# Kernel tuning notes

Measured on AMD Instinct MI355X. Metric: run time of the kernel, lower is better.

Reference implementation:

```python
import jax, jax.numpy as jnp
import numpy as np

D_MODEL = 1024
N_HEADS = 16
N_KV_HEADS = 4
D_K = D_MODEL // N_HEADS
Q_SIZE = D_MODEL
KV_SIZE = N_KV_HEADS * D_K
QKV_SIZE = Q_SIZE + 2 * KV_SIZE
EPS = 1.1920929e-07  # torch.nn.RMSNorm default eps (fp32 machine eps)
ROPE_BASE = 10000.0


def rms_norm(x, w):
    # normalize over last dim, learned scale (torch nn.RMSNorm)
    return x * jax.lax.rsqrt(jnp.mean(x * x, axis=-1, keepdims=True) + EPS) * w


def rope(x):
    # torchtune RotaryPositionalEmbeddings: interleaved pairs, x is [B,T,H,D]
    T, d = x.shape[1], x.shape[-1]
    inv_freq = 1.0 / (ROPE_BASE ** (jnp.arange(0, d, 2, dtype=jnp.float32) / d))
    ang = jnp.arange(T, dtype=jnp.float32)[:, None] * inv_freq[None, :]  # [T, d/2]
    cos = jnp.cos(ang)[None, :, None, :]
    sin = jnp.sin(ang)[None, :, None, :]
    xr = x.reshape(x.shape[:-1] + (d // 2, 2))
    x1, x2 = xr[..., 0], xr[..., 1]
    out = jnp.stack([x1 * cos - x2 * sin, x1 * sin + x2 * cos], axis=-1)
    return out.reshape(x.shape)


def setup_inputs() -> dict:
    key = jax.random.key(0)
    k1, k2 = jax.random.split(key)
    x = jax.random.normal(k1, (2, 2048, D_MODEL), dtype=jnp.float32)
    qkvo = jax.random.normal(k2, (QKV_SIZE + D_MODEL, D_MODEL), dtype=jnp.float32) * 0.02
    q_norm_w = jnp.ones((D_K,), dtype=jnp.float32)
    k_norm_w = jnp.ones((D_K,), dtype=jnp.float32)
    return {"x": x, "qkvo": qkvo, "q_norm_w": q_norm_w, "k_norm_w": k_norm_w}


def reference(x, qkvo, q_norm_w, k_norm_w):
    B, T, _ = x.shape
    groups = N_HEADS // N_KV_HEADS
    qkv = x @ qkvo[:QKV_SIZE].T  # [B,T,qkv_size]
    Q = qkv[..., :Q_SIZE].reshape(B, T, N_HEADS, D_K)
    K = qkv[..., Q_SIZE:Q_SIZE + KV_SIZE].reshape(B, T, N_KV_HEADS, D_K)
    V = qkv[..., Q_SIZE + KV_SIZE:].reshape(B, T, N_KV_HEADS, D_K)
    Q = rope(rms_norm(Q, q_norm_w))
    K = rope(rms_norm(K, k_norm_w))
    K = jnp.repeat(K, groups, axis=2)  # GQA expand to [B,T,H,D]
    V = jnp.repeat(V, groups, axis=2)
    scale = 1.0 / np.sqrt(D_K).astype(np.float32)
    scores = jnp.einsum('bqhd,bkhd->bhqk', Q, K) * scale
    causal = jnp.tril(jnp.ones((T, T), dtype=bool))
    scores = jnp.where(causal[None, None], scores, jnp.float32(-jnp.inf))
    attn = jax.nn.softmax(scores, axis=-1)
    out = jnp.einsum('bhqk,bkhd->bqhd', attn, V).reshape(B, T, D_MODEL)
    return out @ qkvo[QKV_SIZE:].T
```

## Files before the change

### kernel.cpp

```cpp
#include <hip/hip_runtime.h>
#include <hip/hip_bf16.h>
#include <cstdint>
#include <cstddef>

typedef __bf16 bf16x8 __attribute__((ext_vector_type(8)));
typedef float f32x4 __attribute__((ext_vector_type(4)));

__device__ __forceinline__ unsigned short f2bf(float f) {
    unsigned u = __builtin_bit_cast(unsigned, f);
    u += 0x7FFFu + ((u >> 16) & 1u);
    return (unsigned short)(u >> 16);
}
__device__ __forceinline__ unsigned pk2(float a, float b) {
    typedef __bf16 bf16x2 __attribute__((ext_vector_type(2)));
    bf16x2 h;
    h[0] = (__bf16)a;
    h[1] = (__bf16)b;
    unsigned r;
    __builtin_memcpy(&r, &h, 4);
    return r;
}
__device__ __forceinline__ float fexp2(float x) {
#if __has_builtin(__builtin_amdgcn_exp2f)
    return __builtin_amdgcn_exp2f(x);
#else
    return __expf(x * 0.6931471805599453f);
#endif
}
__device__ __forceinline__ void gld16(const void* g, void* l) {
    __builtin_amdgcn_global_load_lds((const __attribute__((address_space(1))) void*)g,
                                     (__attribute__((address_space(3))) void*)l, 16, 0, 0);
}

__global__ __launch_bounds__(256) void cast_kernel(const float4* __restrict__ x,
                                                   const float4* __restrict__ w,
                                                   ushort4* __restrict__ xbf,
                                                   ushort4* __restrict__ wbf) {
    int i = blockIdx.x * 256 + threadIdx.x;
    const int NX4 = 4096 * 1024 / 4;
    const int NW4 = 2560 * 1024 / 4;
    float4 v;
    ushort4* o;
    if (i < NX4) { v = x[i]; o = xbf + i; }
    else {
        int j = i - NX4;
        if (j >= NW4) return;
        v = w[j]; o = wbf + j;
    }
    ushort4 r;
    r.x = f2bf(v.x); r.y = f2bf(v.y); r.z = f2bf(v.z); r.w = f2bf(v.w);
    *o = r;
}

__global__ __launch_bounds__(256) void gemm_bf16(const ushort* __restrict__ A,
                                                 const ushort* __restrict__ B,
                                                 float* __restrict__ C,
                                                 int M, int N, int K) {
    __shared__ __align__(16) ushort LA[2][8192];
    __shared__ __align__(16) ushort LB[2][8192];
    int tid = threadIdx.x;
    int w = tid >> 6, lane = tid & 63;
    int qm = lane & 15, quad = lane >> 4;
    int m0 = blockIdx.x * 128, n0 = blockIdx.y * 128;
    int mw = (w & 1) * 64, nw = (w >> 1) * 64;
    int sw = qm & 7;

    f32x4 acc[4][4];
#pragma unroll
    for (int i = 0; i < 4; i++)
#pragma unroll
        for (int j = 0; j < 4; j++) acc[i][j] = (f32x4){0.f, 0.f, 0.f, 0.f};

    int s[4], rr[4], gg[4];
#pragma unroll
    for (int u = 0; u < 4; u++) {
        s[u] = tid + u * 256;
        rr[u] = s[u] >> 3;
        gg[u] = (s[u] & 7) ^ (rr[u] & 7);
    }

    auto do_stage = [&](int k0, int buf) {
#pragma unroll
        for (int u = 0; u < 4; u++)
            gld16(A + (size_t)(m0 + rr[u]) * K + k0 + gg[u] * 8, &LA[buf][s[u] * 8]);
#pragma unroll
        for (int u = 0; u < 4; u++)
            gld16(B + (size_t)(n0 + rr[u]) * K + k0 + gg[u] * 8, &LB[buf][s[u] * 8]);
    };

    do_stage(0, 0);
    int buf = 0;
    for (int k0 = 0; k0 < K; k0 += 64, buf ^= 1) {
        __syncthreads();
        if (k0 + 64 < K) do_stage(k0 + 64, buf ^ 1);
        bf16x8 a[4][2], bb[4][2];
#pragma unroll
        for (int mi = 0; mi < 4; mi++)
#pragma unroll
            for (int h = 0; h < 2; h++)
                a[mi][h] = *(const bf16x8*)&LA[buf][((mw + mi * 16 + qm) * 8 + ((h * 4 + quad) ^ sw)) * 8];
#pragma unroll
        for (int ni = 0; ni < 4; ni++)
#pragma unroll
            for (int h = 0; h < 2; h++)
                bb[ni][h] = *(const bf16x8*)&LB[buf][((nw + ni * 16 + qm) * 8 + ((h * 4 + quad) ^ sw)) * 8];
#pragma unroll
        for (int h = 0; h < 2; h++)
#pragma unroll
            for (int mi = 0; mi < 4; mi++)
#pragma unroll
                for (int ni = 0; ni < 4; ni++)
                    acc[mi][ni] = __builtin_amdgcn_mfma_f32_16x16x32_bf16(a[mi][h], bb[ni][h], acc[mi][ni], 0, 0, 0);
    }
#pragma unroll
    for (int mi = 0; mi < 4; mi++)
#pragma unroll
        for (int ni = 0; ni < 4; ni++) {
            int row = m0 + mw + mi * 16 + quad * 4;
            int col = n0 + nw + ni * 16 + qm;
            float* cp = C + (size_t)row * N + col;
#pragma unroll
            for (int r = 0; r < 4; r++) cp[(size_t)r * N] = acc[mi][ni][r];
        }
}

__global__ __launch_bounds__(256) void normrope_kernel(const float* __restrict__ qkv,
                                                       const float* __restrict__ qw,
                                                       const float* __restrict__ kw,
                                                       ushort* __restrict__ Q,
                                                       ushort* __restrict__ Kb) {
    int r = blockIdx.x;
    int b = r >> 11;
    int t = r & 2047;
    int tid = threadIdx.x;
    int w = tid >> 6;
    int lane = tid & 63;

    float inv_freq = __expf(-((float)(lane & 62) * (1.0f / 64.0f)) * 9.210340371976184f);
    float sn, cs;
    sincosf((float)t * inv_freq, &sn, &cs);

#pragma unroll
    for (int hg = 0; hg < 5; hg++) {
        int col = hg * 256 + w * 64 + lane;
        float v = qkv[(size_t)r * 1536 + col];
        float ss = v * v;
#pragma unroll
        for (int m = 1; m < 64; m <<= 1) ss += __shfl_xor(ss, m);
        float rinv = rsqrtf(ss * (1.0f / 64.0f) + 1.1920929e-7f);
        float wt = (hg < 4) ? qw[lane] : kw[lane];
        float vn = v * rinv * wt;
        float pr = __shfl_xor(vn, 1);
        float out = (lane & 1) ? fmaf(pr, sn, vn * cs) : fmaf(vn, cs, -pr * sn);
        if (hg < 4) {
            int h = hg * 4 + w;
            Q[((size_t)(b * 16 + h) * 2048 + t) * 64 + lane] = f2bf(out * 0.125f);
        } else {
            Kb[((size_t)(b * 4 + w) * 2048 + t) * 64 + lane] = f2bf(out);
        }
    }
}

__global__ __launch_bounds__(256) void vtrans_kernel(const float* __restrict__ qkv,
                                                     ushort* __restrict__ VT) {
    __shared__ float tile[64][65];
    int bkv = blockIdx.x;
    int t0 = blockIdx.y * 64;
    int b = bkv >> 2;
    int kvh = bkv & 3;
    int tid = threadIdx.x;
    int c = tid & 63;
    int rr = tid >> 6;
#pragma unroll
    for (int p = 0; p < 16; p++) {
        int tl = p * 4 + rr;
        tile[tl][c] = qkv[((size_t)(b * 2048) + t0 + tl) * 1536 + 1280 + kvh * 64 + c];
    }
    __syncthreads();
#pragma unroll
    for (int p = 0; p < 16; p++) {
        int dd = p * 4 + rr;
        VT[((size_t)bkv * 64 + dd) * 2048 + t0 + c] = f2bf(tile[c][dd]);
    }
}

__global__ __launch_bounds__(256) void attn5_kernel(const ushort* __restrict__ Q,
                                                    const ushort* __restrict__ K,
                                                    const ushort* __restrict__ VT,
                                                    ushort* __restrict__ O) {
    __shared__ __align__(16) ushort KT[2][4096];
    __shared__ __align__(16) ushort VL[2][4096];
    __shared__ __align__(16) ushort PBuf[4][1024];

    const float LOG2E = 1.4426950408889634f;
    const float C8 = 11.541560327111707f;

    int blk = blockIdx.x;
    int bh = blk >> 4;
    int p  = blk & 15;
    int tid = threadIdx.x;
    int w = tid >> 6, lane = tid & 63;
    int qm = lane & 15, quad = lane >> 4;
    int b = bh >> 4, h = bh & 15;
    int bkv = b * 4 + (h >> 2);

    const ushort* Qbh = Q + (size_t)bh * 2048 * 64;
    const ushort* Kbh = K + (size_t)bkv * 2048 * 64;
    const ushort* Vbh = VT + (size_t)bkv * 64 * 2048;
    ushort* pb = PBuf[w];
    int sw = qm & 7;

    int s0 = tid, s1 = tid + 256;
    int r0 = s0 >> 3, g0 = (s0 & 7) ^ (r0 & 7);
    int r1 = s1 >> 3, g1 = (s1 & 7) ^ (r1 & 7);

    auto do_stage = [&](int j0, int buf) {
        gld16(Kbh + (size_t)(j0 + r0) * 64 + g0 * 8, &KT[buf][s0 * 8]);
        gld16(Kbh + (size_t)(j0 + r1) * 64 + g1 * 8, &KT[buf][s1 * 8]);
        gld16(Vbh + (size_t)r0 * 2048 + j0 + g0 * 8, &VL[buf][s0 * 8]);
        gld16(Vbh + (size_t)r1 * 2048 + j0 + g1 * 8, &VL[buf][s1 * 8]);
    };

    int qblkA = p, qblkB = 31 - p;
    int nchA = qblkA + 1;
    const int total = 33;

    int q0 = qblkA * 64 + w * 16;
    const ushort* qptr = Qbh + (size_t)(q0 + qm) * 64 + quad * 8;
    bf16x8 qb0 = *(const bf16x8*)qptr;
    bf16x8 qb1 = *(const bf16x8*)(qptr + 32);
    f32x4 oacc[4];
    float lacc = 0.f;
#pragma unroll
    for (int i = 0; i < 4; i++) oacc[i] = (f32x4){0.f, 0.f, 0.f, 0.f};

    auto writeO = [&]() {
        float l = lacc;
        l += __shfl_xor(l, 16);
        l += __shfl_xor(l, 32);
        float rinv = 1.0f / l;
        uint2 val;
#pragma unroll
        for (int dt = 0; dt < 4; dt++) {
            val.x = pk2(oacc[dt][0] * rinv, oacc[dt][1] * rinv);
            val.y = pk2(oacc[dt][2] * rinv, oacc[dt][3] * rinv);
            *(uint2*)&O[((size_t)(b * 2048) + q0 + qm) * 1024 + h * 64 + dt * 16 + quad * 4] = val;
        }
    };

    do_stage(0, 0);
    int buf = 0;
#pragma unroll 1
    for (int i = 0; i < total; i++, buf ^= 1) {
        bool inB = (i >= nchA);
        int c = inB ? i - nchA : i;
        int j0 = c * 64;
        int nch = inB ? (qblkB + 1) : nchA;

        if (i == nchA) {
            writeO();
            q0 = qblkB * 64 + w * 16;
            const ushort* qp2 = Qbh + (size_t)(q0 + qm) * 64 + quad * 8;
            qb0 = *(const bf16x8*)qp2;
            qb1 = *(const bf16x8*)(qp2 + 32);
            lacc = 0.f;
#pragma unroll
            for (int ii = 0; ii < 4; ii++) oacc[ii] = (f32x4){0.f, 0.f, 0.f, 0.f};
        }

        __syncthreads();
        int ni = i + 1;
        if (ni < total) do_stage(ni < nchA ? 64 * ni : 64 * (ni - nchA), buf ^ 1);

        f32x4 st[4];
#pragma unroll
        for (int tj = 0; tj < 4; tj++) st[tj] = (f32x4){0.f, 0.f, 0.f, 0.f};
#pragma unroll
        for (int tj = 0; tj < 4; tj++) {
            bf16x8 kf0 = *(const bf16x8*)&KT[buf][((16 * tj + qm) * 8 + (quad ^ sw)) * 8];
            bf16x8 kf1 = *(const bf16x8*)&KT[buf][((16 * tj + qm) * 8 + ((4 + quad) ^ sw)) * 8];
            st[tj] = __builtin_amdgcn_mfma_f32_16x16x32_bf16(kf0, qb0, st[tj], 0, 0, 0);
            st[tj] = __builtin_amdgcn_mfma_f32_16x16x32_bf16(kf1, qb1, st[tj], 0, 0, 0);
        }
        if (c == nch - 1) {
#pragma unroll
            for (int tj = 0; tj < 4; tj++)
#pragma unroll
                for (int r = 0; r < 4; r++) {
                    int key = j0 + tj * 16 + quad * 4 + r;
                    if (key > q0 + qm) st[tj][r] = -1e30f;
                }
        }
        float rs = 0.f;
#pragma unroll
        for (int tj = 0; tj < 4; tj++)
#pragma unroll
            for (int r = 0; r < 4; r++) {
                float pv = fexp2(fmaf(st[tj][r], LOG2E, -C8));
                st[tj][r] = pv;
                rs += pv;
            }
        lacc += rs;

#pragma unroll
        for (int tj = 0; tj < 4; tj++) {
            int g = 2 * tj + (quad >> 1);
            uint2 val;
            val.x = pk2(st[tj][0], st[tj][1]);
            val.y = pk2(st[tj][2], st[tj][3]);
            *(uint2*)&pb[(qm * 8 + (g ^ sw)) * 8 + (quad & 1) * 4] = val;
        }
        asm volatile("s_waitcnt lgkmcnt(0)" ::: "memory");

#pragma unroll
        for (int half = 0; half < 2; half++) {
            int gg = 4 * half + quad;
            bf16x8 pfrag = *(const bf16x8*)&pb[(qm * 8 + (gg ^ sw)) * 8];
#pragma unroll
            for (int dt = 0; dt < 4; dt++) {
                bf16x8 vf = *(const bf16x8*)&VL[buf][((16 * dt + qm) * 8 + (gg ^ sw)) * 8];
                oacc[dt] = __builtin_amdgcn_mfma_f32_16x16x32_bf16(vf, pfrag, oacc[dt], 0, 0, 0);
            }
        }
    }
    writeO();
}

extern "C" void kernel_launch(void* const* d_in, const int* in_sizes, int n_in,
                              void* d_out, int out_size, void* d_ws, size_t ws_size,
                              hipStream_t stream) {
    (void)in_sizes; (void)n_in; (void)out_size; (void)ws_size;
    const float* x    = (const float*)d_in[0];
    const float* qkvo = (const float*)d_in[1];
    const float* qw   = (const float*)d_in[2];
    const float* kw   = (const float*)d_in[3];
    float* out = (float*)d_out;

    char* ws = (char*)d_ws;
    ushort* xbf = (ushort*)(ws + 0);
    ushort* wbf = (ushort*)(ws + 8388608);
    float*  qkv = (float*)(ws + 13631488);
    ushort* Qb  = (ushort*)(ws + 38797312);
    ushort* Kb  = (ushort*)(ws + 47185920);
    ushort* VT  = (ushort*)(ws + 49283072);
    ushort* Ob  = (ushort*)(ws + 51380224);

    cast_kernel<<<6656, 256, 0, stream>>>((const float4*)x, (const float4*)qkvo,
                                          (ushort4*)xbf, (ushort4*)wbf);
    gemm_bf16<<<dim3(32, 12), 256, 0, stream>>>(xbf, wbf, qkv, 4096, 1536, 1024);
    normrope_kernel<<<4096, 256, 0, stream>>>(qkv, qw, kw, Qb, Kb);
    vtrans_kernel<<<dim3(8, 32), 256, 0, stream>>>(qkv, VT);
    attn5_kernel<<<512, 256, 0, stream>>>(Qb, Kb, VT, Ob);
    gemm_bf16<<<dim3(32, 8), 256, 0, stream>>>(Ob, wbf + (size_t)1536 * 1024, out, 4096, 1024, 1024);
}
```

Before: 171.8 us.

## Shrink GEMM M-tile to 64 and split attention into per-query-block workgroups

```diff
diff --git a/kernel.cpp b/kernel.cpp
--- a/kernel.cpp
+++ b/kernel.cpp
@@ -56,36 +56,43 @@
                                                  const ushort* __restrict__ B,
                                                  float* __restrict__ C,
                                                  int M, int N, int K) {
-    __shared__ __align__(16) ushort LA[2][8192];
+    __shared__ __align__(16) ushort LA[2][4096];
     __shared__ __align__(16) ushort LB[2][8192];
     int tid = threadIdx.x;
     int w = tid >> 6, lane = tid & 63;
     int qm = lane & 15, quad = lane >> 4;
-    int m0 = blockIdx.x * 128, n0 = blockIdx.y * 128;
-    int mw = (w & 1) * 64, nw = (w >> 1) * 64;
+    int m0 = blockIdx.x * 64, n0 = blockIdx.y * 128;
+    int mw = (w & 1) * 32, nw = (w >> 1) * 64;
     int sw = qm & 7;
 
-    f32x4 acc[4][4];
-#pragma unroll
-    for (int i = 0; i < 4; i++)
+    f32x4 acc[2][4];
+#pragma unroll
+    for (int i = 0; i < 2; i++)
 #pragma unroll
         for (int j = 0; j < 4; j++) acc[i][j] = (f32x4){0.f, 0.f, 0.f, 0.f};
 
-    int s[4], rr[4], gg[4];
+    int sa[2], ra[2], ga[2];
+#pragma unroll
+    for (int u = 0; u < 2; u++) {
+        sa[u] = tid + u * 256;
+        ra[u] = sa[u] >> 3;
+        ga[u] = (sa[u] & 7) ^ (ra[u] & 7);
+    }
+    int sb[4], rb[4], gb[4];
 #pragma unroll
     for (int u = 0; u < 4; u++) {
-        s[u] = tid + u * 256;
-        rr[u] = s[u] >> 3;
-        gg[u] = (s[u] & 7) ^ (rr[u] & 7);
+        sb[u] = tid + u * 256;
+        rb[u] = sb[u] >> 3;
+        gb[u] = (sb[u] & 7) ^ (rb[u] & 7);
     }
 
     auto do_stage = [&](int k0, int buf) {
 #pragma unroll
+        for (int u = 0; u < 2; u++)
+            gld16(A + (size_t)(m0 + ra[u]) * K + k0 + ga[u] * 8, &LA[buf][sa[u] * 8]);
+#pragma unroll
         for (int u = 0; u < 4; u++)
-            gld16(A + (size_t)(m0 + rr[u]) * K + k0 + gg[u] * 8, &LA[buf][s[u] * 8]);
-#pragma unroll
-        for (int u = 0; u < 4; u++)
-            gld16(B + (size_t)(n0 + rr[u]) * K + k0 + gg[u] * 8, &LB[buf][s[u] * 8]);
+            gld16(B + (size_t)(n0 + rb[u]) * K + k0 + gb[u] * 8, &LB[buf][sb[u] * 8]);
     };
 
     do_stage(0, 0);
@@ -93,9 +100,9 @@
     for (int k0 = 0; k0 < K; k0 += 64, buf ^= 1) {
         __syncthreads();
         if (k0 + 64 < K) do_stage(k0 + 64, buf ^ 1);
-        bf16x8 a[4][2], bb[4][2];
-#pragma unroll
-        for (int mi = 0; mi < 4; mi++)
+        bf16x8 a[2][2], bb[4][2];
+#pragma unroll
+        for (int mi = 0; mi < 2; mi++)
 #pragma unroll
             for (int h = 0; h < 2; h++)
                 a[mi][h] = *(const bf16x8*)&LA[buf][((mw + mi * 16 + qm) * 8 + ((h * 4 + quad) ^ sw)) * 8];
@@ -107,13 +114,13 @@
 #pragma unroll
         for (int h = 0; h < 2; h++)
 #pragma unroll
-            for (int mi = 0; mi < 4; mi++)
+            for (int mi = 0; mi < 2; mi++)
 #pragma unroll
                 for (int ni = 0; ni < 4; ni++)
                     acc[mi][ni] = __builtin_amdgcn_mfma_f32_16x16x32_bf16(a[mi][h], bb[ni][h], acc[mi][ni], 0, 0, 0);
     }
 #pragma unroll
-    for (int mi = 0; mi < 4; mi++)
+    for (int mi = 0; mi < 2; mi++)
 #pragma unroll
         for (int ni = 0; ni < 4; ni++) {
             int row = m0 + mw + mi * 16 + quad * 4;
@@ -184,7 +191,7 @@
     }
 }
 
-__global__ __launch_bounds__(256) void attn5_kernel(const ushort* __restrict__ Q,
+__global__ __launch_bounds__(256) void attn6_kernel(const ushort* __restrict__ Q,
                                                     const ushort* __restrict__ K,
                                                     const ushort* __restrict__ VT,
                                                     ushort* __restrict__ O) {
@@ -196,8 +203,8 @@
     const float C8 = 11.541560327111707f;
 
     int blk = blockIdx.x;
-    int bh = blk >> 4;
-    int p  = blk & 15;
+    int qp = 31 - (blk >> 5);
+    int bh = blk & 31;
     int tid = threadIdx.x;
     int w = tid >> 6, lane = tid & 63;
     int qm = lane & 15, quad = lane >> 4;
@@ -221,11 +228,8 @@
         gld16(Vbh + (size_t)r1 * 2048 + j0 + g1 * 8, &VL[buf][s1 * 8]);
     };
 
-    int qblkA = p, qblkB = 31 - p;
-    int nchA = qblkA + 1;
-    const int total = 33;
-
-    int q0 = qblkA * 64 + w * 16;
+    int nch = qp + 1;
+    int q0 = qp * 64 + w * 16;
     const ushort* qptr = Qbh + (size_t)(q0 + qm) * 64 + quad * 8;
     bf16x8 qb0 = *(const bf16x8*)qptr;
     bf16x8 qb1 = *(const bf16x8*)(qptr + 32);
@@ -234,43 +238,13 @@
 #pragma unroll
     for (int i = 0; i < 4; i++) oacc[i] = (f32x4){0.f, 0.f, 0.f, 0.f};
 
-    auto writeO = [&]() {
-        float l = lacc;
-        l += __shfl_xor(l, 16);
-        l += __shfl_xor(l, 32);
-        float rinv = 1.0f / l;
-        uint2 val;
-#pragma unroll
-        for (int dt = 0; dt < 4; dt++) {
-            val.x = pk2(oacc[dt][0] * rinv, oacc[dt][1] * rinv);
-            val.y = pk2(oacc[dt][2] * rinv, oacc[dt][3] * rinv);
-            *(uint2*)&O[((size_t)(b * 2048) + q0 + qm) * 1024 + h * 64 + dt * 16 + quad * 4] = val;
-        }
-    };
-
     do_stage(0, 0);
     int buf = 0;
 #pragma unroll 1
-    for (int i = 0; i < total; i++, buf ^= 1) {
-        bool inB = (i >= nchA);
-        int c = inB ? i - nchA : i;
-        int j0 = c * 64;
-        int nch = inB ? (qblkB + 1) : nchA;
-
-        if (i == nchA) {
-            writeO();
-            q0 = qblkB * 64 + w * 16;
-            const ushort* qp2 = Qbh + (size_t)(q0 + qm) * 64 + quad * 8;
-            qb0 = *(const bf16x8*)qp2;
-            qb1 = *(const bf16x8*)(qp2 + 32);
-            lacc = 0.f;
-#pragma unroll
-            for (int ii = 0; ii < 4; ii++) oacc[ii] = (f32x4){0.f, 0.f, 0.f, 0.f};
-        }
-
+    for (int i = 0; i < nch; i++, buf ^= 1) {
+        int j0 = i * 64;
         __syncthreads();
-        int ni = i + 1;
-        if (ni < total) do_stage(ni < nchA ? 64 * ni : 64 * (ni - nchA), buf ^ 1);
+        if (i + 1 < nch) do_stage(j0 + 64, buf ^ 1);
 
         f32x4 st[4];
 #pragma unroll
@@ -282,7 +256,7 @@
             st[tj] = __builtin_amdgcn_mfma_f32_16x16x32_bf16(kf0, qb0, st[tj], 0, 0, 0);
             st[tj] = __builtin_amdgcn_mfma_f32_16x16x32_bf16(kf1, qb1, st[tj], 0, 0, 0);
         }
-        if (c == nch - 1) {
+        if (i == nch - 1) {
 #pragma unroll
             for (int tj = 0; tj < 4; tj++)
 #pragma unroll
@@ -323,7 +297,17 @@
             }
         }
     }
-    writeO();
+    float l = lacc;
+    l += __shfl_xor(l, 16);
+    l += __shfl_xor(l, 32);
+    float rinv = 1.0f / l;
+    uint2 val;
+#pragma unroll
+    for (int dt = 0; dt < 4; dt++) {
+        val.x = pk2(oacc[dt][0] * rinv, oacc[dt][1] * rinv);
+        val.y = pk2(oacc[dt][2] * rinv, oacc[dt][3] * rinv);
+        *(uint2*)&O[((size_t)(b * 2048) + q0 + qm) * 1024 + h * 64 + dt * 16 + quad * 4] = val;
+    }
 }
 
 extern "C" void kernel_launch(void* const* d_in, const int* in_sizes, int n_in,
@@ -347,9 +331,9 @@
 
     cast_kernel<<<6656, 256, 0, stream>>>((const float4*)x, (const float4*)qkvo,
                                           (ushort4*)xbf, (ushort4*)wbf);
-    gemm_bf16<<<dim3(32, 12), 256, 0, stream>>>(xbf, wbf, qkv, 4096, 1536, 1024);
+    gemm_bf16<<<dim3(64, 12), 256, 0, stream>>>(xbf, wbf, qkv, 4096, 1536, 1024);
     normrope_kernel<<<4096, 256, 0, stream>>>(qkv, qw, kw, Qb, Kb);
     vtrans_kernel<<<dim3(8, 32), 256, 0, stream>>>(qkv, VT);
-    attn5_kernel<<<512, 256, 0, stream>>>(Qb, Kb, VT, Ob);
-    gemm_bf16<<<dim3(32, 8), 256, 0, stream>>>(Ob, wbf + (size_t)1536 * 1024, out, 4096, 1024, 1024);
-}
+    attn6_kernel<<<1024, 256, 0, stream>>>(Qb, Kb, VT, Ob);
+    gemm_bf16<<<dim3(64, 8), 256, 0, stream>>>(Ob, wbf + (size_t)1536 * 1024, out, 4096, 1024, 1024);
+}
```

Measured after the change: 159.7 us. -7.0%, faster.
